# Performance work log

Hardware: AMD Instinct MI355X
Metric: run time of the kernel (lower is better)

The kernel has to match this reference:

```python
import jax, jax.numpy as jnp
import numpy as np

D_MODEL = 768
HEAD_SIZE = 64

def setup_inputs() -> dict:
    key = jax.random.key(0)
    ks = jax.random.split(key, 7)
    B, S = 8, 2048
    x = jax.random.normal(ks[0], (B, S, D_MODEL), dtype=jnp.float32)
    s = 1.0 / np.sqrt(D_MODEL)
    Wq = jax.random.uniform(ks[1], (D_MODEL, HEAD_SIZE), jnp.float32, -s, s)
    bq = jnp.zeros((HEAD_SIZE,), jnp.float32)
    Wk = jax.random.uniform(ks[2], (D_MODEL, HEAD_SIZE), jnp.float32, -s, s)
    bk = jnp.zeros((HEAD_SIZE,), jnp.float32)
    Wv = jax.random.uniform(ks[3], (D_MODEL, HEAD_SIZE), jnp.float32, -s, s)
    bv = jnp.zeros((HEAD_SIZE,), jnp.float32)
    return {"x": x, "Wq": Wq, "bq": bq, "Wk": Wk, "bk": bk, "Wv": Wv, "bv": bv}

def reference(x, Wq, bq, Wk, bk, Wv, bv):
    # Single attention head: softmax(Q K^T / sqrt(head_size)) V
    q = jnp.einsum('bsd,dh->bsh', x, Wq) + bq  # [B,S,H]
    k = jnp.einsum('bsd,dh->bsh', x, Wk) + bk
    v = jnp.einsum('bsd,dh->bsh', x, Wv) + bv
    scale = 1.0 / jnp.sqrt(jnp.array(HEAD_SIZE, dtype=x.dtype))
    scores = jnp.einsum('bqh,bkh->bqk', q, k) * scale  # [B,S,S]
    attn = jax.nn.softmax(scores, axis=-1)
    out = jnp.einsum('bqk,bkh->bqh', attn, v)  # [B,S,H]
    return out
```

## Files before the change

### kernel.cpp

```cpp
#include <hip/hip_runtime.h>
#include <math.h>

#define D_MODEL 768
#define HS 64
#define BATCH 8
#define SEQ 2048
#define SCALE 0.125f
#define KSPLIT 8
#define KCHUNK (SEQ / KSPLIT)

typedef _Float16 half_t;
typedef __attribute__((ext_vector_type(8))) _Float16 half8;
typedef __attribute__((ext_vector_type(4))) float floatx4;

typedef const __attribute__((address_space(1))) void gas_void;
typedef __attribute__((address_space(3))) void las_void;
__device__ __forceinline__ void gl_lds16(const void* g, void* l) {
    __builtin_amdgcn_global_load_lds((gas_void*)g, (las_void*)l, 16, 0, 0);
}
__device__ __forceinline__ void waitcnt_all() {
    __builtin_amdgcn_s_waitcnt(0);
}

__global__ __launch_bounds__(256)
void wconv_kernel(const float* __restrict__ Wq, const float* __restrict__ Wk,
                  const float* __restrict__ Wv, half_t* __restrict__ Wt)
{
    int m = blockIdx.x >> 6;
    int h = blockIdx.x & 63;
    const float* W = (m == 0) ? Wq : ((m == 1) ? Wk : Wv);
    half_t* dst = Wt + (size_t)blockIdx.x * D_MODEL;
    for (int k = threadIdx.x; k < D_MODEL; k += 256)
        dst[k] = (half_t)W[(size_t)k * HS + h];
}

__global__ __launch_bounds__(256)
void proj_kernel(const float* __restrict__ x, const half_t* __restrict__ Wt,
                 const float* __restrict__ bq, const float* __restrict__ bk,
                 const float* __restrict__ bv,
                 half_t* __restrict__ Qh, half_t* __restrict__ Kh,
                 half_t* __restrict__ Vt)
{
    __shared__ __align__(16) float  xs[32 * 64];
    __shared__ __align__(16) half_t wt[192 * 64];

    const int tid = threadIdx.x;
    const int w = tid >> 6;
    const int lane = tid & 63;
    const int l15 = lane & 15;
    const int quad = lane >> 4;
    const long row0 = (long)blockIdx.x * 32;

    floatx4 acc[2][3];
#pragma unroll
    for (int i = 0; i < 2; ++i)
#pragma unroll
        for (int j = 0; j < 3; ++j) acc[i][j] = (floatx4){0.f, 0.f, 0.f, 0.f};

    for (int k0 = 0; k0 < D_MODEL; k0 += 64) {
        __syncthreads();
#pragma unroll
        for (int i = 0; i < 2; ++i) {
            int idx = i * 256 + tid;
            int r = idx >> 4, sc = idx & 15;
            int cg = sc ^ (r & 15);
            gl_lds16(x + (row0 + r) * D_MODEL + k0 + cg * 4, xs + idx * 4);
        }
#pragma unroll
        for (int i = 0; i < 6; ++i) {
            int idx = i * 256 + tid;
            int r = idx >> 3, sc = idx & 7;
            int cg = sc ^ (r & 7);
            gl_lds16(Wt + (size_t)r * D_MODEL + k0 + cg * 8, wt + idx * 8);
        }
        waitcnt_all();
        __syncthreads();

#pragma unroll
        for (int kst = 0; kst < 2; ++kst) {
            half8 af[2];
#pragma unroll
            for (int mt = 0; mt < 2; ++mt) {
                int r = mt * 16 + l15;
                int c0 = kst * 8 + quad * 2;
                float4 f0 = *(const float4*)&xs[r * 64 + (c0 ^ l15) * 4];
                float4 f1 = *(const float4*)&xs[r * 64 + ((c0 + 1) ^ l15) * 4];
                af[mt] = (half8){(half_t)f0.x, (half_t)f0.y, (half_t)f0.z, (half_t)f0.w,
                                 (half_t)f1.x, (half_t)f1.y, (half_t)f1.z, (half_t)f1.w};
            }
#pragma unroll
            for (int nt = 0; nt < 3; ++nt) {
                int r = w * 48 + nt * 16 + l15;
                int slot = (kst * 4 + quad) ^ (r & 7);
                half8 bf = *(const half8*)&wt[r * 64 + slot * 8];
#pragma unroll
                for (int mt = 0; mt < 2; ++mt)
                    acc[mt][nt] = __builtin_amdgcn_mfma_f32_16x16x32_f16(
                        af[mt], bf, acc[mt][nt], 0, 0, 0);
            }
        }
    }

#pragma unroll
    for (int nt = 0; nt < 3; ++nt) {
        int nbase = w * 48 + nt * 16;
        int mm = nbase >> 6;
        int h = (nbase + l15) & 63;
        const float* bias = (mm == 0) ? bq : ((mm == 1) ? bk : bv);
        float bval = bias[h];
#pragma unroll
        for (int mt = 0; mt < 2; ++mt)
#pragma unroll
            for (int r = 0; r < 4; ++r) {
                long R = row0 + mt * 16 + quad * 4 + r;
                half_t hv = (half_t)(acc[mt][nt][r] + bval);
                if (mm == 0)      Qh[R * HS + h] = hv;
                else if (mm == 1) Kh[R * HS + h] = hv;
                else {
                    long bb = R >> 11, s = R & 2047;
                    Vt[(bb * HS + h) * SEQ + s] = hv;
                }
            }
    }
}

__global__ __launch_bounds__(256)
void attn_kernel(const half_t* __restrict__ Qh, const half_t* __restrict__ Kh,
                 const half_t* __restrict__ Vt,
                 half_t* __restrict__ Opart, float* __restrict__ lpart)
{
    __shared__ __align__(16) half_t ks[64 * 64];
    __shared__ __align__(16) half_t vs[64 * 64];
    __shared__ __align__(16) half_t ps[4][16][72];

    const int tid = threadIdx.x;
    const int w = tid >> 6;
    const int lane = tid & 63;
    const int l15 = lane & 15;
    const int quad = lane >> 4;
    const int b = blockIdx.y;
    const int q0 = blockIdx.x * 256 + w * 64;
    const int kh = blockIdx.z;
    const int kk_begin = kh * KCHUNK;

    const half_t* Kb = Kh + (size_t)b * SEQ * HS;
    const half_t* Vb = Vt + (size_t)b * HS * SEQ;

    half8 qf[4][2];
#pragma unroll
    for (int mt = 0; mt < 4; ++mt)
#pragma unroll
        for (int kst = 0; kst < 2; ++kst) {
            half8 q = *(const half8*)(Qh + ((size_t)b * SEQ + q0 + mt * 16 + l15) * HS
                                      + kst * 32 + quad * 8);
#pragma unroll
            for (int j = 0; j < 8; ++j) q[j] = q[j] * (half_t)SCALE;
            qf[mt][kst] = q;
        }

    floatx4 oacc[4][4];
    float lsum[4][4];
#pragma unroll
    for (int mt = 0; mt < 4; ++mt) {
#pragma unroll
        for (int nt = 0; nt < 4; ++nt) oacc[mt][nt] = (floatx4){0.f, 0.f, 0.f, 0.f};
#pragma unroll
        for (int r = 0; r < 4; ++r) lsum[mt][r] = 0.f;
    }

    for (int it = 0; it < KCHUNK / 64; ++it) {
        const int kk0 = kk_begin + it * 64;
        __syncthreads();
#pragma unroll
        for (int i = 0; i < 2; ++i) {
            int idx = i * 256 + tid;
            int r = idx >> 3, sc = idx & 7;
            int cg = sc ^ (r & 7);
            gl_lds16(Kb + (size_t)(kk0 + r) * HS + cg * 8, ks + idx * 8);
            gl_lds16(Vb + (size_t)r * SEQ + kk0 + cg * 8, vs + idx * 8);
        }
        waitcnt_all();
        __syncthreads();

        half8 vf[4][2];
#pragma unroll
        for (int nt = 0; nt < 4; ++nt)
#pragma unroll
            for (int kst = 0; kst < 2; ++kst) {
                int r = nt * 16 + l15;
                int slot = (kst * 4 + quad) ^ (r & 7);
                vf[nt][kst] = *(const half8*)&vs[r * 64 + slot * 8];
            }

#pragma unroll
        for (int h2 = 0; h2 < 2; ++h2) {
            floatx4 sacc[2][4];
#pragma unroll
            for (int mtl = 0; mtl < 2; ++mtl)
#pragma unroll
                for (int nt = 0; nt < 4; ++nt) sacc[mtl][nt] = (floatx4){0.f, 0.f, 0.f, 0.f};
#pragma unroll
            for (int nt = 0; nt < 4; ++nt)
#pragma unroll
                for (int kst = 0; kst < 2; ++kst) {
                    int r = nt * 16 + l15;
                    int slot = (kst * 4 + quad) ^ (r & 7);
                    half8 kf = *(const half8*)&ks[r * 64 + slot * 8];
#pragma unroll
                    for (int mtl = 0; mtl < 2; ++mtl)
                        sacc[mtl][nt] = __builtin_amdgcn_mfma_f32_16x16x32_f16(
                            qf[h2 * 2 + mtl][kst], kf, sacc[mtl][nt], 0, 0, 0);
                }

#pragma unroll
            for (int mtl = 0; mtl < 2; ++mtl) {
                int mt = h2 * 2 + mtl;
#pragma unroll
                for (int nt = 0; nt < 4; ++nt)
#pragma unroll
                    for (int r = 0; r < 4; ++r) {
                        float pv = __expf(sacc[mtl][nt][r]);
                        lsum[mt][r] += pv;
                        ps[w][quad * 4 + r][nt * 16 + l15] = (half_t)pv;
                    }
                half8 pfr[2];
#pragma unroll
                for (int kst = 0; kst < 2; ++kst)
                    pfr[kst] = *(const half8*)&ps[w][l15][kst * 32 + quad * 8];
#pragma unroll
                for (int nt = 0; nt < 4; ++nt)
#pragma unroll
                    for (int kst = 0; kst < 2; ++kst)
                        oacc[mt][nt] = __builtin_amdgcn_mfma_f32_16x16x32_f16(
                            pfr[kst], vf[nt][kst], oacc[mt][nt], 0, 0, 0);
            }
        }
    }

#pragma unroll
    for (int mt = 0; mt < 4; ++mt)
#pragma unroll
        for (int r = 0; r < 4; ++r) {
            float s = lsum[mt][r];
            s += __shfl_xor(s, 1);
            s += __shfl_xor(s, 2);
            s += __shfl_xor(s, 4);
            s += __shfl_xor(s, 8);
            lsum[mt][r] = s;
        }

    size_t obase = ((size_t)kh * BATCH + b) * SEQ * HS;
#pragma unroll
    for (int mt = 0; mt < 4; ++mt)
#pragma unroll
        for (int nt = 0; nt < 4; ++nt)
#pragma unroll
            for (int r = 0; r < 4; ++r) {
                int row = q0 + mt * 16 + quad * 4 + r;
                Opart[obase + (size_t)row * HS + nt * 16 + l15] = (half_t)oacc[mt][nt][r];
            }
    if (l15 == 0) {
#pragma unroll
        for (int mt = 0; mt < 4; ++mt)
#pragma unroll
            for (int r = 0; r < 4; ++r) {
                int row = q0 + mt * 16 + quad * 4 + r;
                lpart[((size_t)kh * BATCH + b) * SEQ + row] = lsum[mt][r];
            }
    }
}

__global__ __launch_bounds__(256)
void combine_kernel(const half_t* __restrict__ Opart, const float* __restrict__ lpart,
                    float* __restrict__ out)
{
    const size_t NT = (size_t)BATCH * SEQ * HS;
    const size_t BS = (size_t)BATCH * SEQ;
    size_t e0 = ((size_t)blockIdx.x * 256 + threadIdx.x) * 8;
    size_t row = e0 / HS;
    float o[8] = {0, 0, 0, 0, 0, 0, 0, 0};
    float l = 0.f;
#pragma unroll
    for (int i = 0; i < KSPLIT; ++i) {
        half8 oi = *(const half8*)(Opart + (size_t)i * NT + e0);
#pragma unroll
        for (int j = 0; j < 8; ++j) o[j] += (float)oi[j];
        l += lpart[(size_t)i * BS + row];
    }
    float inv = 1.f / l;
    float4 a = {o[0] * inv, o[1] * inv, o[2] * inv, o[3] * inv};
    float4 c = {o[4] * inv, o[5] * inv, o[6] * inv, o[7] * inv};
    *(float4*)(out + e0) = a;
    *(float4*)(out + e0 + 4) = c;
}

extern "C" void kernel_launch(void* const* d_in, const int* in_sizes, int n_in,
                              void* d_out, int out_size, void* d_ws, size_t ws_size,
                              hipStream_t stream) {
    const float* x  = (const float*)d_in[0];
    const float* Wq = (const float*)d_in[1];
    const float* bq = (const float*)d_in[2];
    const float* Wk = (const float*)d_in[3];
    const float* bk = (const float*)d_in[4];
    const float* Wv = (const float*)d_in[5];
    const float* bv = (const float*)d_in[6];
    float* out = (float*)d_out;

    const size_t per = (size_t)BATCH * SEQ * HS;
    half_t* Qh = (half_t*)d_ws;
    half_t* Kh = Qh + per;
    half_t* Vt = Kh + per;
    half_t* Wt = Vt + per;
    half_t* Opart = Wt + 3 * HS * D_MODEL;
    float*  lpart = (float*)(Opart + (size_t)KSPLIT * per);

    wconv_kernel<<<dim3(3 * HS), dim3(256), 0, stream>>>(Wq, Wk, Wv, Wt);
    proj_kernel<<<dim3(BATCH * SEQ / 32), dim3(256), 0, stream>>>(
        x, Wt, bq, bk, bv, Qh, Kh, Vt);
    attn_kernel<<<dim3(SEQ / 256, BATCH, KSPLIT), dim3(256), 0, stream>>>(
        Qh, Kh, Vt, Opart, lpart);
    combine_kernel<<<dim3((BATCH * SEQ * HS) / (256 * 8)), dim3(256), 0, stream>>>(
        Opart, lpart, out);
}
```

Measured before the change: 141.8 us.

## Register-prefetch double-buffered projection with larger row tile; shrink attention blocks

```diff
diff --git a/kernel.cpp b/kernel.cpp
--- a/kernel.cpp
+++ b/kernel.cpp
@@ -41,64 +41,90 @@
                  half_t* __restrict__ Qh, half_t* __restrict__ Kh,
                  half_t* __restrict__ Vt)
 {
-    __shared__ __align__(16) float  xs[32 * 64];
-    __shared__ __align__(16) half_t wt[192 * 64];
+    __shared__ __align__(16) half_t xs[2][64 * 64];
+    __shared__ __align__(16) half_t wt[2][192 * 64];
 
     const int tid = threadIdx.x;
     const int w = tid >> 6;
     const int lane = tid & 63;
     const int l15 = lane & 15;
     const int quad = lane >> 4;
-    const long row0 = (long)blockIdx.x * 32;
-
-    floatx4 acc[2][3];
-#pragma unroll
-    for (int i = 0; i < 2; ++i)
+    const long row0 = (long)blockIdx.x * 64;
+
+    floatx4 acc[4][3];
+#pragma unroll
+    for (int i = 0; i < 4; ++i)
 #pragma unroll
         for (int j = 0; j < 3; ++j) acc[i][j] = (floatx4){0.f, 0.f, 0.f, 0.f};
 
-    for (int k0 = 0; k0 < D_MODEL; k0 += 64) {
-        __syncthreads();
+    float4 xA[4], xB[4];
+    half8  wA[6], wB[6];
+
+    auto loadx = [&](int k0, float4 (&v)[4]) {
 #pragma unroll
         for (int i = 0; i < 2; ++i) {
             int idx = i * 256 + tid;
-            int r = idx >> 4, sc = idx & 15;
-            int cg = sc ^ (r & 15);
-            gl_lds16(x + (row0 + r) * D_MODEL + k0 + cg * 4, xs + idx * 4);
-        }
+            int r = idx >> 3, sc = idx & 7;
+            int cg = sc ^ (r & 7);
+            const float* p = x + (row0 + r) * D_MODEL + k0 + cg * 8;
+            v[i * 2]     = *(const float4*)p;
+            v[i * 2 + 1] = *(const float4*)(p + 4);
+        }
+    };
+    auto loadw = [&](int k0, half8 (&wr)[6]) {
 #pragma unroll
         for (int i = 0; i < 6; ++i) {
             int idx = i * 256 + tid;
             int r = idx >> 3, sc = idx & 7;
             int cg = sc ^ (r & 7);
-            gl_lds16(Wt + (size_t)r * D_MODEL + k0 + cg * 8, wt + idx * 8);
-        }
-        waitcnt_all();
+            wr[i] = *(const half8*)(Wt + (size_t)r * D_MODEL + k0 + cg * 8);
+        }
+    };
+
+    auto step = [&](int it, float4 (&xc)[4], half8 (&wc)[6],
+                    float4 (&xn)[4], half8 (&wn)[6], int p) {
+#pragma unroll
+        for (int i = 0; i < 2; ++i) {
+            float4 a = xc[i * 2], b = xc[i * 2 + 1];
+            half8 xh = (half8){(half_t)a.x, (half_t)a.y, (half_t)a.z, (half_t)a.w,
+                               (half_t)b.x, (half_t)b.y, (half_t)b.z, (half_t)b.w};
+            *(half8*)&xs[p][(i * 256 + tid) * 8] = xh;
+        }
+#pragma unroll
+        for (int i = 0; i < 6; ++i)
+            *(half8*)&wt[p][(i * 256 + tid) * 8] = wc[i];
         __syncthreads();
-
+        int kn = (it + 1 < 12) ? (it + 1) * 64 : 0;
+        loadx(kn, xn);
+        loadw(kn, wn);
 #pragma unroll
         for (int kst = 0; kst < 2; ++kst) {
-            half8 af[2];
-#pragma unroll
-            for (int mt = 0; mt < 2; ++mt) {
+            half8 af[4];
+#pragma unroll
+            for (int mt = 0; mt < 4; ++mt) {
                 int r = mt * 16 + l15;
-                int c0 = kst * 8 + quad * 2;
-                float4 f0 = *(const float4*)&xs[r * 64 + (c0 ^ l15) * 4];
-                float4 f1 = *(const float4*)&xs[r * 64 + ((c0 + 1) ^ l15) * 4];
-                af[mt] = (half8){(half_t)f0.x, (half_t)f0.y, (half_t)f0.z, (half_t)f0.w,
-                                 (half_t)f1.x, (half_t)f1.y, (half_t)f1.z, (half_t)f1.w};
+                int slot = (kst * 4 + quad) ^ (r & 7);
+                af[mt] = *(const half8*)&xs[p][r * 64 + slot * 8];
             }
 #pragma unroll
             for (int nt = 0; nt < 3; ++nt) {
                 int r = w * 48 + nt * 16 + l15;
                 int slot = (kst * 4 + quad) ^ (r & 7);
-                half8 bf = *(const half8*)&wt[r * 64 + slot * 8];
-#pragma unroll
-                for (int mt = 0; mt < 2; ++mt)
+                half8 bf = *(const half8*)&wt[p][r * 64 + slot * 8];
+#pragma unroll
+                for (int mt = 0; mt < 4; ++mt)
                     acc[mt][nt] = __builtin_amdgcn_mfma_f32_16x16x32_f16(
                         af[mt], bf, acc[mt][nt], 0, 0, 0);
             }
         }
+    };
+
+    loadx(0, xA);
+    loadw(0, wA);
+#pragma unroll
+    for (int it = 0; it < 12; it += 2) {
+        step(it,     xA, wA, xB, wB, 0);
+        step(it + 1, xB, wB, xA, wA, 1);
     }
 
 #pragma unroll
@@ -109,7 +135,7 @@
         const float* bias = (mm == 0) ? bq : ((mm == 1) ? bk : bv);
         float bval = bias[h];
 #pragma unroll
-        for (int mt = 0; mt < 2; ++mt)
+        for (int mt = 0; mt < 4; ++mt)
 #pragma unroll
             for (int r = 0; r < 4; ++r) {
                 long R = row0 + mt * 16 + quad * 4 + r;
@@ -124,14 +150,14 @@
     }
 }
 
-__global__ __launch_bounds__(256)
+__global__ __launch_bounds__(128)
 void attn_kernel(const half_t* __restrict__ Qh, const half_t* __restrict__ Kh,
                  const half_t* __restrict__ Vt,
                  half_t* __restrict__ Opart, float* __restrict__ lpart)
 {
     __shared__ __align__(16) half_t ks[64 * 64];
     __shared__ __align__(16) half_t vs[64 * 64];
-    __shared__ __align__(16) half_t ps[4][16][72];
+    __shared__ __align__(16) half_t ps[2][16][72];
 
     const int tid = threadIdx.x;
     const int w = tid >> 6;
@@ -139,7 +165,7 @@
     const int l15 = lane & 15;
     const int quad = lane >> 4;
     const int b = blockIdx.y;
-    const int q0 = blockIdx.x * 256 + w * 64;
+    const int q0 = blockIdx.x * 128 + w * 64;
     const int kh = blockIdx.z;
     const int kk_begin = kh * KCHUNK;
 
@@ -172,8 +198,8 @@
         const int kk0 = kk_begin + it * 64;
         __syncthreads();
 #pragma unroll
-        for (int i = 0; i < 2; ++i) {
-            int idx = i * 256 + tid;
+        for (int i = 0; i < 4; ++i) {
+            int idx = i * 128 + tid;
             int r = idx >> 3, sc = idx & 7;
             int cg = sc ^ (r & 7);
             gl_lds16(Kb + (size_t)(kk0 + r) * HS + cg * 8, ks + idx * 8);
@@ -315,9 +341,9 @@
     float*  lpart = (float*)(Opart + (size_t)KSPLIT * per);
 
     wconv_kernel<<<dim3(3 * HS), dim3(256), 0, stream>>>(Wq, Wk, Wv, Wt);
-    proj_kernel<<<dim3(BATCH * SEQ / 32), dim3(256), 0, stream>>>(
+    proj_kernel<<<dim3(BATCH * SEQ / 64), dim3(256), 0, stream>>>(
         x, Wt, bq, bk, bv, Qh, Kh, Vt);
-    attn_kernel<<<dim3(SEQ / 256, BATCH, KSPLIT), dim3(256), 0, stream>>>(
+    attn_kernel<<<dim3(SEQ / 128, BATCH, KSPLIT), dim3(128), 0, stream>>>(
         Qh, Kh, Vt, Opart, lpart);
     combine_kernel<<<dim3((BATCH * SEQ * HS) / (256 * 8)), dim3(256), 0, stream>>>(
         Opart, lpart, out);
```

Measured after the change: 141.2 us. Within noise of the previous version (-0.4%).
